# Optimization experiments

Measured on AMD Instinct MI355X. Metric: run time of the kernel, lower is better.

The kernel has to match this reference:

```python
import jax, jax.numpy as jnp
import numpy as np

V, LAG, H, M, O, B = 32, 1024, 512, 1024, 1, 256


def setup_inputs() -> dict:
    key = jax.random.key(0)
    ks = jax.random.split(key, 10)
    s_ih = 1.0 / np.sqrt(H)
    inputs = jax.random.normal(ks[0], (B, V, LAG, 1), dtype=jnp.float32)
    # per-variable LSTMCell params, stacked over vars; gate order i,f,g,o (torch)
    W_ih = jax.random.uniform(ks[1], (V, 4 * H, LAG), minval=-s_ih, maxval=s_ih, dtype=jnp.float32)
    W_hh = jax.random.uniform(ks[2], (V, 4 * H, H), minval=-s_ih, maxval=s_ih, dtype=jnp.float32)
    b_ih = jax.random.uniform(ks[3], (V, 4 * H), minval=-s_ih, maxval=s_ih, dtype=jnp.float32)
    b_hh = jax.random.uniform(ks[4], (V, 4 * H), minval=-s_ih, maxval=s_ih, dtype=jnp.float32)
    imp_weights = jnp.asarray(np.ones((V,), np.float32) / V + np.random.RandomState(0).normal(0, 1e-5, (V,)).astype(np.float32))
    # xavier-normal linears, bias 0.1 (init_weights)
    mlp1_w = jax.random.normal(ks[5], (M, V * H), dtype=jnp.float32) * np.sqrt(2.0 / (V * H + M))
    mlp1_b = jnp.full((M,), 0.1, dtype=jnp.float32)
    mlp2_w = jax.random.normal(ks[6], (O, M), dtype=jnp.float32) * np.sqrt(2.0 / (M + O))
    mlp2_b = jnp.full((O,), 0.1, dtype=jnp.float32)
    return dict(inputs=inputs, W_ih=W_ih, W_hh=W_hh, b_ih=b_ih, b_hh=b_hh,
                imp_weights=imp_weights, mlp1_w=mlp1_w, mlp1_b=mlp1_b,
                mlp2_w=mlp2_w, mlp2_b=mlp2_b)


def reference(inputs, W_ih, W_hh, b_ih, b_hh, imp_weights, mlp1_w, mlp1_b, mlp2_w, mlp2_b):
    b = inputs.shape[0]
    x = inputs.reshape(b, V, LAG)                      # [B,V,LAG] (view in torch)
    h0 = jnp.zeros((b, V, H), inputs.dtype)           # initial states are zeros
    # single LSTMCell step for all vars at once; gate order i,f,g,o
    gates = (jnp.einsum('bvl,vgl->bvg', x, W_ih)
             + jnp.einsum('bvh,vgh->bvg', h0, W_hh)
             + b_ih[None] + b_hh[None])                # [B,V,4H]
    i, f, g, o = jnp.split(gates, 4, axis=-1)
    c = jax.nn.sigmoid(f) * 0.0 + jax.nn.sigmoid(i) * jnp.tanh(g)  # c0 = 0
    # original aggregates the CELL state (lstm_state[1]) weighted per variable
    agg = (c * imp_weights[None, :, None]).reshape(b, V * H)
    hid = jax.nn.relu(agg @ mlp1_w.T + mlp1_b)
    return hid @ mlp2_w.T + mlp2_b
```

## Files before the change

kernel.cpp:

```cpp
#include <hip/hip_runtime.h>
#include <hip/hip_bf16.h>
#include <stdint.h>

#define NVAR 32
#define LAGD 1024
#define BATCH 256
#define HDIM 512
#define SPLIT 16

typedef __attribute__((ext_vector_type(4))) float f32x4;
typedef __attribute__((ext_vector_type(8))) short short8;
typedef __attribute__((ext_vector_type(4))) unsigned short us4;
typedef __attribute__((ext_vector_type(8))) unsigned short us8;

__device__ __forceinline__ unsigned short f2bf(float f) {
  union { __hip_bfloat16 b; unsigned short s; } cv;
  cv.b = __float2bfloat16(f);
  return cv.s;
}
__device__ __forceinline__ us8 cvt8(f32x4 a, f32x4 b) {
  us8 u;
#pragma unroll
  for (int e = 0; e < 4; ++e) { u[e] = f2bf(a[e]); u[4 + e] = f2bf(b[e]); }
  return u;
}
__device__ __forceinline__ us4 cvt4(f32x4 a) {
  us4 u;
#pragma unroll
  for (int e = 0; e < 4; ++e) u[e] = f2bf(a[e]);
  return u;
}

__device__ __forceinline__ void gload16(const void* g, const void* l) {
  __builtin_amdgcn_global_load_lds(
      (const __attribute__((address_space(1))) unsigned int*)(uintptr_t)g,
      (__attribute__((address_space(3))) unsigned int*)(unsigned int)(uintptr_t)l,
      16, 0, 0);
}

__device__ __forceinline__ f32x4 gldx4(const float* p) {
  f32x4 r;
  asm volatile("global_load_dwordx4 %0, %1, off" : "=v"(r) : "v"(p) : "memory");
  return r;
}

#define WAITVM(N) do { \
    asm volatile("s_waitcnt vmcnt(" #N ")" ::: "memory"); \
    __builtin_amdgcn_sched_barrier(0); } while (0)

__device__ __forceinline__ void sync_ds() {
  asm volatile("s_waitcnt lgkmcnt(0)" ::: "memory");
  __builtin_amdgcn_s_barrier();
}

__global__ __launch_bounds__(512, 4) void k1_gates(
    const float* __restrict__ X,
    const float* __restrict__ W,
    const float* __restrict__ b_ih,
    const float* __restrict__ b_hh,
    const float* __restrict__ imp,
    unsigned short* __restrict__ aggT)
{
  const int bid = blockIdx.x;
  const int chunk = ((bid & 7) << 6) | (bid >> 3);
  const int v = chunk >> 4;
  const int h0 = (chunk & 15) << 5;

  const int t = threadIdx.x, lane = t & 63, wave = t >> 6;
  const int wm = wave & 3, wh = wave >> 2;

  __shared__ __align__(16) unsigned char smem[81920];

  const int rt = t >> 3, c8 = (t & 7) << 3;
  const float* Asrc = X + (size_t)rt * (NVAR * LAGD) + (size_t)v * LAGD + c8;
  const unsigned awoff = (unsigned)(((rt << 7) + (c8 << 1)) ^ ((rt & 7) << 4));

  const int brow = t >> 3;
  const int wrow = (brow < 32) ? (h0 + brow) : (1024 + h0 + brow - 32);
  const float* Bsrc = W + (size_t)v * (2048 * LAGD) + (size_t)wrow * LAGD + ((t & 7) << 3);
  const unsigned bwoff = (unsigned)(((brow << 7) + ((t & 7) << 4)) ^ ((brow & 7) << 4));

  f32x4 acc_i[4] = {}, acc_g[4] = {};
  f32x4 pa[4][2], pbA[2], pbB[2];

#define ALOAD(KT) do { \
    _Pragma("unroll") for (int _p = 0; _p < 4; ++_p) { \
      pa[_p][0] = gldx4(Asrc + (size_t)_p * 64 * (NVAR * LAGD) + (KT) * 64); \
      pa[_p][1] = gldx4(Asrc + (size_t)_p * 64 * (NVAR * LAGD) + (KT) * 64 + 4); \
    } } while (0)

#define ASTORE(BUF) do { \
    _Pragma("unroll") for (int _p = 0; _p < 4; ++_p) \
      *(us8*)(smem + (BUF) * 32768u + awoff + _p * 8192u) = cvt8(pa[_p][0], pa[_p][1]); \
  } while (0)

#define BLOAD(PB, KT) do { \
    (PB)[0] = gldx4(Bsrc + (KT) * 64); \
    (PB)[1] = gldx4(Bsrc + (KT) * 64 + 4); } while (0)

#define BSTORE(BUF, PB) \
    *(us8*)(smem + 65536u + (BUF) * 8192u + bwoff) = cvt8((PB)[0], (PB)[1])

#define COMP(BUF) do { \
    const unsigned char* Ab = smem + (BUF) * 32768u; \
    const unsigned char* Bb = smem + 65536u + (BUF) * 8192u; \
    const int fr = lane & 15, k16 = (lane >> 4) << 4; \
    _Pragma("unroll") for (int kk = 0; kk < 2; ++kk) { \
      short8 a[4], fi, fg; \
      _Pragma("unroll") for (int i = 0; i < 4; ++i) { \
        const int rw = (wm << 6) + (i << 4) + fr; \
        a[i] = *(const short8*)(Ab + (((rw << 7) + (kk << 6) + k16) ^ ((rw & 7) << 4))); \
      } \
      { const int rw = (wh << 4) + fr; \
        fi = *(const short8*)(Bb + (((rw << 7) + (kk << 6) + k16) ^ ((rw & 7) << 4))); \
        fg = *(const short8*)(Bb + ((((rw + 32) << 7) + (kk << 6) + k16) ^ ((rw & 7) << 4))); } \
      _Pragma("unroll") for (int i = 0; i < 4; ++i) { \
        acc_i[i] = __builtin_amdgcn_mfma_f32_16x16x32_bf16(a[i], fi, acc_i[i], 0, 0, 0); \
        acc_g[i] = __builtin_amdgcn_mfma_f32_16x16x32_bf16(a[i], fg, acc_g[i], 0, 0, 0); } \
    } } while (0)

#define STEP(CUR, NXT, PBP, PBN, KT) do { \
    ALOAD((KT) + 1);         \
    BLOAD(PBN, (KT) + 2);    \
    COMP(CUR); \
    WAITVM(2);    \
    ASTORE(NXT); \
    BSTORE(NXT, PBP); \
    sync_ds(); } while (0)

  ALOAD(0);
  BLOAD(pbA, 0);
  BLOAD(pbB, 1);
  WAITVM(2);
  ASTORE(0);
  BSTORE(0, pbA);
  sync_ds();

#pragma unroll
  for (int kt = 0; kt < 14; kt += 2) {
    STEP(0, 1, pbB, pbA, kt);
    STEP(1, 0, pbA, pbB, kt + 1);
  }
  ALOAD(15);
  COMP(0);
  WAITVM(0);
  ASTORE(1);
  BSTORE(1, pbB);
  sync_ds();
  COMP(1);

  const int col16 = lane & 15, row4 = (lane >> 4) << 2;
  const float impv = imp[v];
  const int h = h0 + (wh << 4) + col16;
  const float bsi = b_ih[v * 2048 + h] + b_hh[v * 2048 + h];
  const float bsg = b_ih[v * 2048 + 1024 + h] + b_hh[v * 2048 + 1024 + h];
  char* obase = (char*)aggT + ((size_t)v * 8 + (h >> 6)) * 32768;
  const int hc = h & 63;
#pragma unroll
  for (int i = 0; i < 4; ++i)
#pragma unroll
    for (int r = 0; r < 4; ++r) {
      const int m = (wm << 6) + (i << 4) + row4 + r;
      const float ii = acc_i[i][r] + bsi;
      const float gg = acc_g[i][r] + bsg;
      const float c = (1.0f / (1.0f + __expf(-ii))) * tanhf(gg) * impv;
      *(unsigned short*)(obase + (((m << 7) + (hc << 1)) ^ ((m & 7) << 4))) = f2bf(c);
    }
#undef STEP
#undef COMP
#undef ALOAD
#undef ASTORE
#undef BLOAD
#undef BSTORE
}

__global__ __launch_bounds__(512, 4) void k3_mlp1(
    const unsigned short* __restrict__ aggT,
    const float* __restrict__ Wm,
    unsigned short* __restrict__ part)
{
  const int bid = blockIdx.x;
  const int chunk = ((bid & 7) << 6) | (bid >> 3);
  const int s = chunk >> 5;
  const int n0 = (chunk & 31) << 5;

  const int t = threadIdx.x, lane = t & 63, wave = t >> 6;
  const int wm = wave & 3, wn = wave >> 2;

  __shared__ __align__(16) unsigned char smem[73728];

  const char* Asrc = (const char*)aggT + (size_t)s * 16 * 32768 + wave * 1024 + lane * 16;
  const unsigned aoff = wave * 1024u;

  const int brow = t >> 4;
  const int bcol = (t & 15) << 2;
  const float* Bsrc = Wm + (size_t)(n0 + brow) * 16384 + (size_t)s * 1024 + bcol;
  const unsigned bwoff = (unsigned)(((brow << 7) + (bcol << 1)) ^ ((brow & 7) << 4));

  f32x4 acc[4] = {};
  f32x4 pbA, pbB;

#define GLA(BUF, KT) do { \
    _Pragma("unroll") for (int _r = 0; _r < 4; ++_r) \
      gload16(Asrc + (KT) * 32768 + _r * 8192, \
              smem + (BUF) * 32768u + aoff + _r * 8192); } while (0)

#define BLOAD(PB, KT) (PB) = gldx4(Bsrc + (KT) * 64)

#define BSTORE(BUF, PB) \
    *(us4*)(smem + 65536u + (BUF) * 4096u + bwoff) = cvt4(PB)

#define COMP(BUF) do { \
    const unsigned char* Ab = smem + (BUF) * 32768u; \
    const unsigned char* Bb = smem + 65536u + (BUF) * 4096u; \
    const int fr = lane & 15, k16 = (lane >> 4) << 4; \
    _Pragma("unroll") for (int kk = 0; kk < 2; ++kk) { \
      short8 a[4], bfr; \
      _Pragma("unroll") for (int i = 0; i < 4; ++i) { \
        const int rw = (wm << 6) + (i << 4) + fr; \
        a[i] = *(const short8*)(Ab + (((rw << 7) + (kk << 6) + k16) ^ ((rw & 7) << 4))); \
      } \
      { const int rw = (wn << 4) + fr; \
        bfr = *(const short8*)(Bb + (((rw << 7) + (kk << 6) + k16) ^ ((rw & 7) << 4))); } \
      _Pragma("unroll") for (int i = 0; i < 4; ++i) \
        acc[i] = __builtin_amdgcn_mfma_f32_16x16x32_bf16(a[i], bfr, acc[i], 0, 0, 0); \
    } } while (0)

#define STEP(CUR, NXT, PBP, PBN, KT) do { \
    GLA(NXT, (KT) + 1);      \
    BLOAD(PBN, (KT) + 2);    \
    COMP(CUR); \
    WAITVM(1);    \
    BSTORE(NXT, PBP); \
    sync_ds(); } while (0)

  GLA(0, 0);
  BLOAD(pbA, 0);
  BLOAD(pbB, 1);
  WAITVM(1);
  BSTORE(0, pbA);
  sync_ds();

#pragma unroll
  for (int kt = 0; kt < 14; kt += 2) {
    STEP(0, 1, pbB, pbA, kt);
    STEP(1, 0, pbA, pbB, kt + 1);
  }
  GLA(1, 15);
  COMP(0);
  WAITVM(0);
  BSTORE(1, pbB);
  sync_ds();
  COMP(1);

  const int col16 = lane & 15, row4 = (lane >> 4) << 2;
  unsigned short* outp = part + (size_t)s * BATCH * 1024;
#pragma unroll
  for (int i = 0; i < 4; ++i)
#pragma unroll
    for (int r = 0; r < 4; ++r)
      outp[(size_t)((wm << 6) + (i << 4) + row4 + r) * 1024
           + n0 + (wn << 4) + col16] = f2bf(acc[i][r]);
#undef STEP
#undef COMP
#undef GLA
#undef BLOAD
#undef BSTORE
}

__global__ __launch_bounds__(512) void k4_head(
    const unsigned short* __restrict__ part,
    const float* __restrict__ b1,
    const float* __restrict__ w2,
    const float* __restrict__ b2,
    float* __restrict__ out)
{
  const int b = blockIdx.x;
  const int t = threadIdx.x;
  const int n0 = t << 1;
  float s0 = b1[n0], s1 = b1[n0 + 1];
#pragma unroll
  for (int sp = 0; sp < SPLIT; ++sp) {
    const unsigned u = *(const unsigned*)(part + ((size_t)sp * BATCH + b) * 1024 + n0);
    union { unsigned u; float f; } lo, hi;
    lo.u = u << 16;
    hi.u = u & 0xffff0000u;
    s0 += lo.f;
    s1 += hi.f;
  }
  float accum = fmaxf(s0, 0.0f) * w2[n0] + fmaxf(s1, 0.0f) * w2[n0 + 1];
  __shared__ float red[8];
#pragma unroll
  for (int off = 32; off > 0; off >>= 1)
    accum += __shfl_down(accum, off);
  if ((t & 63) == 0) red[t >> 6] = accum;
  __syncthreads();
  if (t == 0) {
    float r = b2[0];
#pragma unroll
    for (int w = 0; w < 8; ++w) r += red[w];
    out[b] = r;
  }
}

extern "C" void kernel_launch(void* const* d_in, const int* in_sizes, int n_in,
                              void* d_out, int out_size, void* d_ws, size_t ws_size,
                              hipStream_t stream) {
  const float* inputs = (const float*)d_in[0];
  const float* W_ih   = (const float*)d_in[1];
  const float* b_ih   = (const float*)d_in[3];
  const float* b_hh   = (const float*)d_in[4];
  const float* imp    = (const float*)d_in[5];
  const float* m1w    = (const float*)d_in[6];
  const float* m1b    = (const float*)d_in[7];
  const float* m2w    = (const float*)d_in[8];
  const float* m2b    = (const float*)d_in[9];
  float* out = (float*)d_out;

  char* ws = (char*)d_ws;
  unsigned short* aggT = (unsigned short*)ws;
  unsigned short* part = (unsigned short*)(ws + (8u << 20));

  k1_gates<<<dim3(512), 512, 0, stream>>>(inputs, W_ih, b_ih, b_hh, imp, aggT);
  k3_mlp1 <<<dim3(512), 512, 0, stream>>>(aggT, m1w, part);
  k4_head <<<dim3(256), 512, 0, stream>>>(part, m1b, m2w, m2b, out);
}
```

Measured before the change: 69.21 us.

## Load weight tiles in 4-k-tile groups with larger per-thread reads, halve occupancy

Result: slower. 109.3 us (+57.9%).

```diff
diff --git a/kernel.cpp b/kernel.cpp
--- a/kernel.cpp
+++ b/kernel.cpp
@@ -24,12 +24,6 @@
   for (int e = 0; e < 4; ++e) { u[e] = f2bf(a[e]); u[4 + e] = f2bf(b[e]); }
   return u;
 }
-__device__ __forceinline__ us4 cvt4(f32x4 a) {
-  us4 u;
-#pragma unroll
-  for (int e = 0; e < 4; ++e) u[e] = f2bf(a[e]);
-  return u;
-}
 
 __device__ __forceinline__ void gload16(const void* g, const void* l) {
   __builtin_amdgcn_global_load_lds(
@@ -44,8 +38,8 @@
   return r;
 }
 
-#define WAITVM(N) do { \
-    asm volatile("s_waitcnt vmcnt(" #N ")" ::: "memory"); \
+#define WAITVM0() do { \
+    asm volatile("s_waitcnt vmcnt(0)" ::: "memory"); \
     __builtin_amdgcn_sched_barrier(0); } while (0)
 
 __device__ __forceinline__ void sync_ds() {
@@ -53,7 +47,7 @@
   __builtin_amdgcn_s_barrier();
 }
 
-__global__ __launch_bounds__(512, 4) void k1_gates(
+__global__ __launch_bounds__(512, 2) void k1_gates(
     const float* __restrict__ X,
     const float* __restrict__ W,
     const float* __restrict__ b_ih,
@@ -69,7 +63,7 @@
   const int t = threadIdx.x, lane = t & 63, wave = t >> 6;
   const int wm = wave & 3, wh = wave >> 2;
 
-  __shared__ __align__(16) unsigned char smem[81920];
+  __shared__ __align__(16) unsigned char smem[131072];
 
   const int rt = t >> 3, c8 = (t & 7) << 3;
   const float* Asrc = X + (size_t)rt * (NVAR * LAGD) + (size_t)v * LAGD + c8;
@@ -77,11 +71,12 @@
 
   const int brow = t >> 3;
   const int wrow = (brow < 32) ? (h0 + brow) : (1024 + h0 + brow - 32);
-  const float* Bsrc = W + (size_t)v * (2048 * LAGD) + (size_t)wrow * LAGD + ((t & 7) << 3);
-  const unsigned bwoff = (unsigned)(((brow << 7) + ((t & 7) << 4)) ^ ((brow & 7) << 4));
+  const float* Bsrc = W + (size_t)v * (2048 * LAGD) + (size_t)wrow * LAGD + ((t & 7) << 5);
+  const unsigned btile = (unsigned)((t & 7) >> 1);
+  const unsigned bkb   = (unsigned)(((t & 7) & 1) << 6);
 
   f32x4 acc_i[4] = {}, acc_g[4] = {};
-  f32x4 pa[4][2], pbA[2], pbB[2];
+  f32x4 pa[4][2], pb[8];
 
 #define ALOAD(KT) do { \
     _Pragma("unroll") for (int _p = 0; _p < 4; ++_p) { \
@@ -94,16 +89,19 @@
       *(us8*)(smem + (BUF) * 32768u + awoff + _p * 8192u) = cvt8(pa[_p][0], pa[_p][1]); \
   } while (0)
 
-#define BLOAD(PB, KT) do { \
-    (PB)[0] = gldx4(Bsrc + (KT) * 64); \
-    (PB)[1] = gldx4(Bsrc + (KT) * 64 + 4); } while (0)
-
-#define BSTORE(BUF, PB) \
-    *(us8*)(smem + 65536u + (BUF) * 8192u + bwoff) = cvt8((PB)[0], (PB)[1])
-
-#define COMP(BUF) do { \
-    const unsigned char* Ab = smem + (BUF) * 32768u; \
-    const unsigned char* Bb = smem + 65536u + (BUF) * 8192u; \
+#define BGLOAD(G) do { \
+    _Pragma("unroll") for (int _e = 0; _e < 8; ++_e) \
+      pb[_e] = gldx4(Bsrc + (size_t)(G) * 256 + _e * 4); } while (0)
+
+#define BGSTORE(REG) do { \
+    _Pragma("unroll") for (int _j = 0; _j < 4; ++_j) \
+      *(us8*)(smem + 65536u + (REG) * 32768u + btile * 8192u + \
+              (((brow << 7) + (bkb + (_j << 4))) ^ ((brow & 7) << 4))) \
+          = cvt8(pb[2 * _j], pb[2 * _j + 1]); } while (0)
+
+#define COMP(ABUF, BREG, KTL) do { \
+    const unsigned char* Ab = smem + (ABUF) * 32768u; \
+    const unsigned char* Bb = smem + 65536u + (BREG) * 32768u + (KTL) * 8192u; \
     const int fr = lane & 15, k16 = (lane >> 4) << 4; \
     _Pragma("unroll") for (int kk = 0; kk < 2; ++kk) { \
       short8 a[4], fi, fg; \
@@ -119,35 +117,23 @@
         acc_g[i] = __builtin_amdgcn_mfma_f32_16x16x32_bf16(a[i], fg, acc_g[i], 0, 0, 0); } \
     } } while (0)
 
-#define STEP(CUR, NXT, PBP, PBN, KT) do { \
-    ALOAD((KT) + 1);         \
-    BLOAD(PBN, (KT) + 2);    \
-    COMP(CUR); \
-    WAITVM(2);    \
-    ASTORE(NXT); \
-    BSTORE(NXT, PBP); \
-    sync_ds(); } while (0)
-
+  BGLOAD(0);
   ALOAD(0);
-  BLOAD(pbA, 0);
-  BLOAD(pbB, 1);
-  WAITVM(2);
+  WAITVM0();
+  BGSTORE(0);
   ASTORE(0);
-  BSTORE(0, pbA);
   sync_ds();
 
 #pragma unroll
-  for (int kt = 0; kt < 14; kt += 2) {
-    STEP(0, 1, pbB, pbA, kt);
-    STEP(1, 0, pbA, pbB, kt + 1);
+  for (int kt = 0; kt < 16; ++kt) {
+    if (kt < 15) ALOAD(kt + 1);
+    COMP(kt & 1, (kt >> 2) & 1, kt & 3);
+    WAITVM0();
+    if (kt < 15) ASTORE((kt + 1) & 1);
+    if ((kt & 3) == 3 && kt < 15) BGSTORE(((kt >> 2) + 1) & 1);
+    if ((kt & 3) == 0 && kt < 12) BGLOAD((kt >> 2) + 1);
+    sync_ds();
   }
-  ALOAD(15);
-  COMP(0);
-  WAITVM(0);
-  ASTORE(1);
-  BSTORE(1, pbB);
-  sync_ds();
-  COMP(1);
 
   const int col16 = lane & 15, row4 = (lane >> 4) << 2;
   const float impv = imp[v];
@@ -166,15 +152,14 @@
       const float c = (1.0f / (1.0f + __expf(-ii))) * tanhf(gg) * impv;
       *(unsigned short*)(obase + (((m << 7) + (hc << 1)) ^ ((m & 7) << 4))) = f2bf(c);
     }
-#undef STEP
 #undef COMP
 #undef ALOAD
 #undef ASTORE
-#undef BLOAD
-#undef BSTORE
-}
-
-__global__ __launch_bounds__(512, 4) void k3_mlp1(
+#undef BGLOAD
+#undef BGSTORE
+}
+
+__global__ __launch_bounds__(512, 2) void k3_mlp1(
     const unsigned short* __restrict__ aggT,
     const float* __restrict__ Wm,
     unsigned short* __restrict__ part)
@@ -187,32 +172,37 @@
   const int t = threadIdx.x, lane = t & 63, wave = t >> 6;
   const int wm = wave & 3, wn = wave >> 2;
 
-  __shared__ __align__(16) unsigned char smem[73728];
+  __shared__ __align__(16) unsigned char smem[98304];
 
   const char* Asrc = (const char*)aggT + (size_t)s * 16 * 32768 + wave * 1024 + lane * 16;
   const unsigned aoff = wave * 1024u;
 
   const int brow = t >> 4;
-  const int bcol = (t & 15) << 2;
-  const float* Bsrc = Wm + (size_t)(n0 + brow) * 16384 + (size_t)s * 1024 + bcol;
-  const unsigned bwoff = (unsigned)(((brow << 7) + (bcol << 1)) ^ ((brow & 7) << 4));
+  const float* Bsrc = Wm + (size_t)(n0 + brow) * 16384 + (size_t)s * 1024 + ((t & 15) << 4);
+  const unsigned btile = (unsigned)((t & 15) >> 2);
+  const unsigned bkb   = (unsigned)(((t & 15) & 3) << 5);
 
   f32x4 acc[4] = {};
-  f32x4 pbA, pbB;
+  f32x4 pb[4];
 
 #define GLA(BUF, KT) do { \
     _Pragma("unroll") for (int _r = 0; _r < 4; ++_r) \
       gload16(Asrc + (KT) * 32768 + _r * 8192, \
               smem + (BUF) * 32768u + aoff + _r * 8192); } while (0)
 
-#define BLOAD(PB, KT) (PB) = gldx4(Bsrc + (KT) * 64)
-
-#define BSTORE(BUF, PB) \
-    *(us4*)(smem + 65536u + (BUF) * 4096u + bwoff) = cvt4(PB)
-
-#define COMP(BUF) do { \
-    const unsigned char* Ab = smem + (BUF) * 32768u; \
-    const unsigned char* Bb = smem + 65536u + (BUF) * 4096u; \
+#define BGLOAD(G) do { \
+    _Pragma("unroll") for (int _e = 0; _e < 4; ++_e) \
+      pb[_e] = gldx4(Bsrc + (size_t)(G) * 256 + _e * 4); } while (0)
+
+#define BGSTORE(REG) do { \
+    _Pragma("unroll") for (int _j = 0; _j < 2; ++_j) \
+      *(us8*)(smem + 65536u + (REG) * 16384u + btile * 4096u + \
+              (((brow << 7) + (bkb + (_j << 4))) ^ ((brow & 7) << 4))) \
+          = cvt8(pb[2 * _j], pb[2 * _j + 1]); } while (0)
+
+#define COMP(ABUF, BREG, KTL) do { \
+    const unsigned char* Ab = smem + (ABUF) * 32768u; \
+    const unsigned char* Bb = smem + 65536u + (BREG) * 16384u + (KTL) * 4096u; \
     const int fr = lane & 15, k16 = (lane >> 4) << 4; \
     _Pragma("unroll") for (int kk = 0; kk < 2; ++kk) { \
       short8 a[4], bfr; \
@@ -226,32 +216,21 @@
         acc[i] = __builtin_amdgcn_mfma_f32_16x16x32_bf16(a[i], bfr, acc[i], 0, 0, 0); \
     } } while (0)
 
-#define STEP(CUR, NXT, PBP, PBN, KT) do { \
-    GLA(NXT, (KT) + 1);      \
-    BLOAD(PBN, (KT) + 2);    \
-    COMP(CUR); \
-    WAITVM(1);    \
-    BSTORE(NXT, PBP); \
-    sync_ds(); } while (0)
-
+  BGLOAD(0);
   GLA(0, 0);
-  BLOAD(pbA, 0);
-  BLOAD(pbB, 1);
-  WAITVM(1);
-  BSTORE(0, pbA);
+  WAITVM0();
+  BGSTORE(0);
   sync_ds();
 
 #pragma unroll
-  for (int kt = 0; kt < 14; kt += 2) {
-    STEP(0, 1, pbB, pbA, kt);
-    STEP(1, 0, pbA, pbB, kt + 1);
+  for (int kt = 0; kt < 16; ++kt) {
+    if (kt < 15) GLA((kt + 1) & 1, kt + 1);
+    COMP(kt & 1, (kt >> 2) & 1, kt & 3);
+    WAITVM0();
+    if ((kt & 3) == 3 && kt < 15) BGSTORE(((kt >> 2) + 1) & 1);
+    if ((kt & 3) == 0 && kt < 12) BGLOAD((kt >> 2) + 1);
+    sync_ds();
   }
-  GLA(1, 15);
-  COMP(0);
-  WAITVM(0);
-  BSTORE(1, pbB);
-  sync_ds();
-  COMP(1);
 
   const int col16 = lane & 15, row4 = (lane >> 4) << 2;
   unsigned short* outp = part + (size_t)s * BATCH * 1024;
@@ -261,11 +240,10 @@
     for (int r = 0; r < 4; ++r)
       outp[(size_t)((wm << 6) + (i << 4) + row4 + r) * 1024
            + n0 + (wn << 4) + col16] = f2bf(acc[i][r]);
-#undef STEP
 #undef COMP
 #undef GLA
-#undef BLOAD
-#undef BSTORE
+#undef BGLOAD
+#undef BGSTORE
 }
 
 __global__ __launch_bounds__(512) void k4_head(
```

## Halve batch tile in gates and MLP1 kernels to double grid size

Applied to the files above, without the earlier changes.

New measurement: 85.01 us. 1.23x slower.

```diff
diff --git a/kernel.cpp b/kernel.cpp
--- a/kernel.cpp
+++ b/kernel.cpp
@@ -53,7 +53,7 @@
   __builtin_amdgcn_s_barrier();
 }
 
-__global__ __launch_bounds__(512, 4) void k1_gates(
+__global__ __launch_bounds__(512, 6) void k1_gates(
     const float* __restrict__ X,
     const float* __restrict__ W,
     const float* __restrict__ b_ih,
@@ -62,59 +62,58 @@
     unsigned short* __restrict__ aggT)
 {
   const int bid = blockIdx.x;
-  const int chunk = ((bid & 7) << 6) | (bid >> 3);
-  const int v = chunk >> 4;
-  const int h0 = (chunk & 15) << 5;
+  const int chunk = ((bid & 7) << 7) | (bid >> 3);
+  const int v  = chunk >> 5;
+  const int h0 = ((chunk & 31) >> 1) << 5;
+  const int mh = chunk & 1;
 
   const int t = threadIdx.x, lane = t & 63, wave = t >> 6;
   const int wm = wave & 3, wh = wave >> 2;
 
-  __shared__ __align__(16) unsigned char smem[81920];
-
-  const int rt = t >> 3, c8 = (t & 7) << 3;
-  const float* Asrc = X + (size_t)rt * (NVAR * LAGD) + (size_t)v * LAGD + c8;
-  const unsigned awoff = (unsigned)(((rt << 7) + (c8 << 1)) ^ ((rt & 7) << 4));
+  __shared__ __align__(16) unsigned char smem[49152];
+
+  const int rt = t >> 2, c16 = (t & 3) << 4;
+  const float* Asrc = X + (size_t)(mh * 128 + rt) * (NVAR * LAGD) + (size_t)v * LAGD + c16;
+  const unsigned aw0 = (unsigned)(((rt << 7) + (c16 << 1)) ^ ((rt & 7) << 4));
+  const unsigned aw1 = (unsigned)(((rt << 7) + (c16 << 1) + 16) ^ ((rt & 7) << 4));
 
   const int brow = t >> 3;
   const int wrow = (brow < 32) ? (h0 + brow) : (1024 + h0 + brow - 32);
   const float* Bsrc = W + (size_t)v * (2048 * LAGD) + (size_t)wrow * LAGD + ((t & 7) << 3);
   const unsigned bwoff = (unsigned)(((brow << 7) + ((t & 7) << 4)) ^ ((brow & 7) << 4));
 
-  f32x4 acc_i[4] = {}, acc_g[4] = {};
-  f32x4 pa[4][2], pbA[2], pbB[2];
+  f32x4 acc_i[2] = {}, acc_g[2] = {};
+  f32x4 pa[4], pbA[2], pbB[2];
 
 #define ALOAD(KT) do { \
-    _Pragma("unroll") for (int _p = 0; _p < 4; ++_p) { \
-      pa[_p][0] = gldx4(Asrc + (size_t)_p * 64 * (NVAR * LAGD) + (KT) * 64); \
-      pa[_p][1] = gldx4(Asrc + (size_t)_p * 64 * (NVAR * LAGD) + (KT) * 64 + 4); \
-    } } while (0)
+    _Pragma("unroll") for (int _e = 0; _e < 4; ++_e) \
+      pa[_e] = gldx4(Asrc + (KT) * 64 + _e * 4); } while (0)
 
 #define ASTORE(BUF) do { \
-    _Pragma("unroll") for (int _p = 0; _p < 4; ++_p) \
-      *(us8*)(smem + (BUF) * 32768u + awoff + _p * 8192u) = cvt8(pa[_p][0], pa[_p][1]); \
-  } while (0)
+    *(us8*)(smem + (BUF) * 16384u + aw0) = cvt8(pa[0], pa[1]); \
+    *(us8*)(smem + (BUF) * 16384u + aw1) = cvt8(pa[2], pa[3]); } while (0)
 
 #define BLOAD(PB, KT) do { \
     (PB)[0] = gldx4(Bsrc + (KT) * 64); \
     (PB)[1] = gldx4(Bsrc + (KT) * 64 + 4); } while (0)
 
 #define BSTORE(BUF, PB) \
-    *(us8*)(smem + 65536u + (BUF) * 8192u + bwoff) = cvt8((PB)[0], (PB)[1])
+    *(us8*)(smem + 32768u + (BUF) * 8192u + bwoff) = cvt8((PB)[0], (PB)[1])
 
 #define COMP(BUF) do { \
-    const unsigned char* Ab = smem + (BUF) * 32768u; \
-    const unsigned char* Bb = smem + 65536u + (BUF) * 8192u; \
+    const unsigned char* Ab = smem + (BUF) * 16384u; \
+    const unsigned char* Bb = smem + 32768u + (BUF) * 8192u; \
     const int fr = lane & 15, k16 = (lane >> 4) << 4; \
     _Pragma("unroll") for (int kk = 0; kk < 2; ++kk) { \
-      short8 a[4], fi, fg; \
-      _Pragma("unroll") for (int i = 0; i < 4; ++i) { \
-        const int rw = (wm << 6) + (i << 4) + fr; \
+      short8 a[2], fi, fg; \
+      _Pragma("unroll") for (int i = 0; i < 2; ++i) { \
+        const int rw = (wm << 5) + (i << 4) + fr; \
         a[i] = *(const short8*)(Ab + (((rw << 7) + (kk << 6) + k16) ^ ((rw & 7) << 4))); \
       } \
       { const int rw = (wh << 4) + fr; \
         fi = *(const short8*)(Bb + (((rw << 7) + (kk << 6) + k16) ^ ((rw & 7) << 4))); \
         fg = *(const short8*)(Bb + ((((rw + 32) << 7) + (kk << 6) + k16) ^ ((rw & 7) << 4))); } \
-      _Pragma("unroll") for (int i = 0; i < 4; ++i) { \
+      _Pragma("unroll") for (int i = 0; i < 2; ++i) { \
         acc_i[i] = __builtin_amdgcn_mfma_f32_16x16x32_bf16(a[i], fi, acc_i[i], 0, 0, 0); \
         acc_g[i] = __builtin_amdgcn_mfma_f32_16x16x32_bf16(a[i], fg, acc_g[i], 0, 0, 0); } \
     } } while (0)
@@ -157,10 +156,10 @@
   char* obase = (char*)aggT + ((size_t)v * 8 + (h >> 6)) * 32768;
   const int hc = h & 63;
 #pragma unroll
-  for (int i = 0; i < 4; ++i)
+  for (int i = 0; i < 2; ++i)
 #pragma unroll
     for (int r = 0; r < 4; ++r) {
-      const int m = (wm << 6) + (i << 4) + row4 + r;
+      const int m = (mh << 7) + (wm << 5) + (i << 4) + row4 + r;
       const float ii = acc_i[i][r] + bsi;
       const float gg = acc_g[i][r] + bsg;
       const float c = (1.0f / (1.0f + __expf(-ii))) * tanhf(gg) * impv;
@@ -174,55 +173,56 @@
 #undef BSTORE
 }
 
-__global__ __launch_bounds__(512, 4) void k3_mlp1(
+__global__ __launch_bounds__(512, 8) void k3_mlp1(
     const unsigned short* __restrict__ aggT,
     const float* __restrict__ Wm,
     unsigned short* __restrict__ part)
 {
   const int bid = blockIdx.x;
-  const int chunk = ((bid & 7) << 6) | (bid >> 3);
-  const int s = chunk >> 5;
-  const int n0 = (chunk & 31) << 5;
+  const int chunk = ((bid & 7) << 7) | (bid >> 3);
+  const int s  = chunk >> 6;
+  const int n0 = ((chunk & 63) >> 1) << 5;
+  const int mh = chunk & 1;
 
   const int t = threadIdx.x, lane = t & 63, wave = t >> 6;
   const int wm = wave & 3, wn = wave >> 2;
 
-  __shared__ __align__(16) unsigned char smem[73728];
-
-  const char* Asrc = (const char*)aggT + (size_t)s * 16 * 32768 + wave * 1024 + lane * 16;
-  const unsigned aoff = wave * 1024u;
+  __shared__ __align__(16) unsigned char smem[40960];
+
+  const char* Asrc = (const char*)aggT + (size_t)s * 16 * 32768 + mh * 16384
+                     + wave * 2048 + lane * 16;
 
   const int brow = t >> 4;
   const int bcol = (t & 15) << 2;
   const float* Bsrc = Wm + (size_t)(n0 + brow) * 16384 + (size_t)s * 1024 + bcol;
   const unsigned bwoff = (unsigned)(((brow << 7) + (bcol << 1)) ^ ((brow & 7) << 4));
 
-  f32x4 acc[4] = {};
+  f32x4 acc[2] = {};
   f32x4 pbA, pbB;
 
 #define GLA(BUF, KT) do { \
-    _Pragma("unroll") for (int _r = 0; _r < 4; ++_r) \
-      gload16(Asrc + (KT) * 32768 + _r * 8192, \
-              smem + (BUF) * 32768u + aoff + _r * 8192); } while (0)
+    _Pragma("unroll") for (int _r = 0; _r < 2; ++_r) \
+      gload16(Asrc + (KT) * 32768 + _r * 1024, \
+              smem + (BUF) * 16384u + wave * 2048u + _r * 1024u); } while (0)
 
 #define BLOAD(PB, KT) (PB) = gldx4(Bsrc + (KT) * 64)
 
 #define BSTORE(BUF, PB) \
-    *(us4*)(smem + 65536u + (BUF) * 4096u + bwoff) = cvt4(PB)
+    *(us4*)(smem + 32768u + (BUF) * 4096u + bwoff) = cvt4(PB)
 
 #define COMP(BUF) do { \
-    const unsigned char* Ab = smem + (BUF) * 32768u; \
-    const unsigned char* Bb = smem + 65536u + (BUF) * 4096u; \
+    const unsigned char* Ab = smem + (BUF) * 16384u; \
+    const unsigned char* Bb = smem + 32768u + (BUF) * 4096u; \
     const int fr = lane & 15, k16 = (lane >> 4) << 4; \
     _Pragma("unroll") for (int kk = 0; kk < 2; ++kk) { \
-      short8 a[4], bfr; \
-      _Pragma("unroll") for (int i = 0; i < 4; ++i) { \
-        const int rw = (wm << 6) + (i << 4) + fr; \
+      short8 a[2], bfr; \
+      _Pragma("unroll") for (int i = 0; i < 2; ++i) { \
+        const int rw = (wm << 5) + (i << 4) + fr; \
         a[i] = *(const short8*)(Ab + (((rw << 7) + (kk << 6) + k16) ^ ((rw & 7) << 4))); \
       } \
       { const int rw = (wn << 4) + fr; \
         bfr = *(const short8*)(Bb + (((rw << 7) + (kk << 6) + k16) ^ ((rw & 7) << 4))); } \
-      _Pragma("unroll") for (int i = 0; i < 4; ++i) \
+      _Pragma("unroll") for (int i = 0; i < 2; ++i) \
         acc[i] = __builtin_amdgcn_mfma_f32_16x16x32_bf16(a[i], bfr, acc[i], 0, 0, 0); \
     } } while (0)
 
@@ -256,10 +256,10 @@
   const int col16 = lane & 15, row4 = (lane >> 4) << 2;
   unsigned short* outp = part + (size_t)s * BATCH * 1024;
 #pragma unroll
-  for (int i = 0; i < 4; ++i)
+  for (int i = 0; i < 2; ++i)
 #pragma unroll
     for (int r = 0; r < 4; ++r)
-      outp[(size_t)((wm << 6) + (i << 4) + row4 + r) * 1024
+      outp[(size_t)((mh << 7) + (wm << 5) + (i << 4) + row4 + r) * 1024
            + n0 + (wn << 4) + col16] = f2bf(acc[i][r]);
 #undef STEP
 #undef COMP
@@ -321,7 +321,7 @@
   unsigned short* aggT = (unsigned short*)ws;
   unsigned short* part = (unsigned short*)(ws + (8u << 20));
 
-  k1_gates<<<dim3(512), 512, 0, stream>>>(inputs, W_ih, b_ih, b_hh, imp, aggT);
-  k3_mlp1 <<<dim3(512), 512, 0, stream>>>(aggT, m1w, part);
+  k1_gates<<<dim3(1024), 512, 0, stream>>>(inputs, W_ih, b_ih, b_hh, imp, aggT);
+  k3_mlp1 <<<dim3(1024), 512, 0, stream>>>(aggT, m1w, part);
   k4_head <<<dim3(256), 512, 0, stream>>>(part, m1b, m2w, m2b, out);
 }
```
